# Performance work log

Measured on AMD Instinct MI355X. Metric: run time of the kernel, lower is better.

The kernel has to match this reference:

```python
import jax, jax.numpy as jnp
import numpy as np
from jax import lax

KERNEL = 2  # kernel_size, forced by the (s3-1, s4-1, s5-1) output reshape


def setup_inputs() -> dict:
    key = jax.random.key(0)
    kx, kw = jax.random.split(key)
    x = jax.random.normal(kx, (4, 16, 32, 32, 32), dtype=jnp.float32)
    w = jax.random.normal(kw, (512, 128), dtype=jnp.float32)  # (d1, d2=C*2^3)
    return {"x": x, "w": w}


def _gaussian_kernel(x, w):
    N, C, D, H, W = x.shape
    d1, d2 = w.shape
    # 3D unfold with kernel 2, stride 1, no padding -> (N, C*8, D-1, H-1, W-1)
    patches = lax.conv_general_dilated_patches(
        x,
        filter_shape=(KERNEL, KERNEL, KERNEL),
        window_strides=(1, 1, 1),
        padding='VALID',
    )
    P = (D - 1) * (H - 1) * (W - 1)
    y = patches.reshape(N, d2, P).transpose(0, 2, 1)  # (N, P, d2)
    # sum((y - w)^2) expanded as ||y||^2 - 2 y.w + ||w||^2 to avoid the
    # (N, P, d1, d2) broadcasted difference tensor.
    y_sq = jnp.sum(y * y, axis=-1, keepdims=True)           # (N, P, 1)
    w_sq = jnp.sum(w * w, axis=-1)                          # (d1,)
    cross = jnp.einsum('npd,kd->npk', y, w)                 # (N, P, d1)
    dist = y_sq - 2.0 * cross + w_sq                        # (N, P, d1)
    out = jnp.exp(-dist)
    return out.transpose(0, 2, 1).reshape(N, d1, D - 1, H - 1, W - 1)


def reference(x, w):
    return _gaussian_kernel(x, w)
```

## Files before the change

kernel.cpp:

```cpp
#include <hip/hip_runtime.h>

typedef unsigned short u16;
typedef unsigned char u8;
typedef float f32x4 __attribute__((ext_vector_type(4)));

#define P_OUT 29791
#define PPAD  29824
#define NBAT  4
#define NCH   512
#define KDIM  128

__device__ __forceinline__ unsigned pk4_fp8(float a, float b, float c, float d) {
  int v = __builtin_amdgcn_cvt_pk_fp8_f32(a, b, 0, false);
  v = __builtin_amdgcn_cvt_pk_fp8_f32(c, d, v, true);
  return (unsigned)v;
}

__global__ void prep_kernel(const float* __restrict__ x,
                            const float* __restrict__ w,
                            u8* __restrict__ yb, float* __restrict__ ysq,
                            u8* __restrict__ wb, float* __restrict__ wsq) {
  const int tid = threadIdx.x;
  const int b = blockIdx.x;
  if (b >= 3844) {
    const int g = (b - 3844) * 16 + (tid >> 4);
    const int c = tid & 15;
    const float4* wr = (const float4*)(w + g * 128 + c * 8);
    float4 f0 = wr[0], f1 = wr[1];
    float s = f0.x*f0.x + f0.y*f0.y + f0.z*f0.z + f0.w*f0.w
            + f1.x*f1.x + f1.y*f1.y + f1.z*f1.z + f1.w*f1.w;
#pragma unroll
    for (int m = 1; m < 16; m <<= 1) s += __shfl_xor(s, m, 64);
    uint2 pk;
    pk.x = pk4_fp8(f0.x, f0.y, f0.z, f0.w);
    pk.y = pk4_fp8(f1.x, f1.y, f1.z, f1.w);
    *(uint2*)(wb + g * 128 + c * 8) = pk;
    if (c == 0) wsq[g] = s;
    return;
  }
  __shared__ float xs[16][4][33];
  const int nb = b / 961;
  const int rem = b - nb * 961;
  const int d = rem / 31;
  const int h = rem - d * 31;
  const float* xb = x + ((size_t)nb << 19) + d * 1024 + h * 32;
#pragma unroll
  for (int t = 0; t < 8; ++t) {
    const int e = tid + 256 * t;
    const int c = e >> 7;
    const int r = (e >> 5) & 3;
    const int wv = e & 31;
    xs[c][r][wv] = xb[((size_t)c << 15) + (r >> 1) * 1024 + (r & 1) * 32 + wv];
  }
  __syncthreads();
  const int cs = tid & 15;
  const int wv0 = tid >> 4;
#pragma unroll
  for (int round = 0; round < 2; ++round) {
    const int wv = wv0 + 16 * round;
    if (wv <= 30) {
      const float v0 = xs[cs][0][wv], v1 = xs[cs][0][wv + 1];
      const float v2 = xs[cs][1][wv], v3 = xs[cs][1][wv + 1];
      const float v4 = xs[cs][2][wv], v5 = xs[cs][2][wv + 1];
      const float v6 = xs[cs][3][wv], v7 = xs[cs][3][wv + 1];
      float s = v0*v0 + v1*v1 + v2*v2 + v3*v3 + v4*v4 + v5*v5 + v6*v6 + v7*v7;
#pragma unroll
      for (int m = 1; m < 16; m <<= 1) s += __shfl_xor(s, m, 64);
      const int g = nb * PPAD + d * 961 + h * 31 + wv;
      uint2 pk;
      pk.x = pk4_fp8(v0, v1, v2, v3);
      pk.y = pk4_fp8(v4, v5, v6, v7);
      *(uint2*)(yb + (size_t)g * 128 + cs * 8) = pk;
      if (cs == 0) ysq[g] = s;
    }
  }
}

#define GLDS(g, l) __builtin_amdgcn_global_load_lds(                         \
    (const __attribute__((address_space(1))) unsigned int*)(g),              \
    (__attribute__((address_space(3))) unsigned int*)(l), 16, 0, 0)

__global__ void gauss_gemm_kernel(const u8* __restrict__ yb,
                                  const float* __restrict__ ysq,
                                  const u8* __restrict__ wb,
                                  const float* __restrict__ wsq,
                                  float* __restrict__ out) {
  __shared__ __align__(16) u8 Ws[128 * 128];
  __shared__ __align__(16) u8 Ys[128 * 128];

  const int bid = blockIdx.x;
  const int ct = bid & 3;
  const int pt = (bid >> 2) % 233;
  const int nb = bid / 932;
  const int p0 = pt * 128;
  const int c0 = ct * 128;

  const int tid = threadIdx.x;
  const int wid = tid >> 6;
  const int lane = tid & 63;
  const int quad = lane >> 4;
  const int col = lane & 15;
  const int wch = wid & 1;
  const int wp = wid >> 1;

  const size_t ybase = ((size_t)nb * PPAD + p0) * 128;

#pragma unroll
  for (int t = 0; t < 4; ++t) {
    const int Lb = (wid * 4 + t) * 64;
    const int L = Lb + lane;
    const int row = L >> 3;
    const int jc = (L & 7) ^ (row & 7);
    GLDS(wb + (size_t)(c0 + row) * 128 + jc * 16, &Ws[Lb * 16]);
    GLDS(yb + ybase + (size_t)row * 128 + jc * 16, &Ys[Lb * 16]);
  }

  f32x4 acc[4][4];
#pragma unroll
  for (int i = 0; i < 4; ++i)
#pragma unroll
    for (int j = 0; j < 4; ++j) acc[i][j] = (f32x4){0.f, 0.f, 0.f, 0.f};

  __syncthreads();

  const int c16b = quad >> 1;
  const int hoff = (quad & 1) * 8;
#pragma unroll
  for (int ks = 0; ks < 4; ++ks) {
    long long a[4], b[4];
#pragma unroll
    for (int i = 0; i < 4; ++i) {
      const int rowA = wch * 64 + i * 16 + col;
      const int pa = (ks * 2 + c16b) ^ (rowA & 7);
      a[i] = *(const long long*)&Ws[rowA * 128 + pa * 16 + hoff];
      const int rowB = wp * 64 + i * 16 + col;
      const int pb = (ks * 2 + c16b) ^ (rowB & 7);
      b[i] = *(const long long*)&Ys[rowB * 128 + pb * 16 + hoff];
    }
#pragma unroll
    for (int i = 0; i < 4; ++i)
#pragma unroll
      for (int j = 0; j < 4; ++j)
        acc[i][j] = __builtin_amdgcn_mfma_f32_16x16x32_fp8_fp8(a[i], b[j],
                                                               acc[i][j], 0, 0, 0);
  }

  float ysv[4];
  int pj[4];
#pragma unroll
  for (int j = 0; j < 4; ++j) {
    pj[j] = p0 + wp * 64 + j * 16 + col;
    ysv[j] = ysq[(size_t)nb * PPAD + pj[j]];
  }
#pragma unroll
  for (int i = 0; i < 4; ++i) {
#pragma unroll
    for (int r = 0; r < 4; ++r) {
      const int ch = c0 + wch * 64 + i * 16 + quad * 4 + r;
      const float wsv = wsq[ch];
      float* ob = out + ((size_t)(nb * NCH + ch)) * P_OUT;
#pragma unroll
      for (int j = 0; j < 4; ++j) {
        if (pj[j] < P_OUT) {
          const float dist = ysv[j] - 2.f * acc[i][j][r] + wsv;
          ob[pj[j]] = __expf(-dist);
        }
      }
    }
  }
}

extern "C" void kernel_launch(void* const* d_in, const int* in_sizes, int n_in,
                              void* d_out, int out_size, void* d_ws, size_t ws_size,
                              hipStream_t stream) {
  const float* x = (const float*)d_in[0];
  const float* w = (const float*)d_in[1];
  float* out = (float*)d_out;
  char* ws = (char*)d_ws;
  u8* yb     = (u8*)ws;
  float* ysq = (float*)(ws + 15269888);
  u8* wb     = (u8*)(ws + 15747072);
  float* wsq = (float*)(ws + 15812608);

  prep_kernel<<<3876, 256, 0, stream>>>(x, w, yb, ysq, wb, wsq);
  gauss_gemm_kernel<<<3728, 256, 0, stream>>>(yb, ysq, wb, wsq, out);
}
```

Before: 288.4 us.

## Make GEMM kernel persistent with resident W tile and prefetched Y tiles

Launches a fixed grid of 1024 blocks that loop over the 3728 output tiles. Each block keeps its W channel tile in LDS for all of its tiles, since the channel tile index is fixed per block. It issues the next Y tile's async global-to-LDS load before running the exp/store epilogue of the current tile. A separate unguarded store path handles full tiles. This aims to cut repeated W loads and block launch overhead and to hide Y load latency behind output stores, but it reduces the number of resident blocks available to keep the memory system busy.

```diff
diff --git a/kernel.cpp b/kernel.cpp
--- a/kernel.cpp
+++ b/kernel.cpp
@@ -9,6 +9,8 @@
 #define NBAT  4
 #define NCH   512
 #define KDIM  128
+#define NTILE 3728
+#define GRID  1024
 
 __device__ __forceinline__ unsigned pk4_fp8(float a, float b, float c, float d) {
   int v = __builtin_amdgcn_cvt_pk_fp8_f32(a, b, 0, false);
@@ -89,12 +91,6 @@
   __shared__ __align__(16) u8 Ys[128 * 128];
 
   const int bid = blockIdx.x;
-  const int ct = bid & 3;
-  const int pt = (bid >> 2) % 233;
-  const int nb = bid / 932;
-  const int p0 = pt * 128;
-  const int c0 = ct * 128;
-
   const int tid = threadIdx.x;
   const int wid = tid >> 6;
   const int lane = tid & 63;
@@ -103,7 +99,8 @@
   const int wch = wid & 1;
   const int wp = wid >> 1;
 
-  const size_t ybase = ((size_t)nb * PPAD + p0) * 128;
+  const int ct = bid & 3;
+  const int c0 = ct * 128;
 
 #pragma unroll
   for (int t = 0; t < 4; ++t) {
@@ -112,61 +109,118 @@
     const int row = L >> 3;
     const int jc = (L & 7) ^ (row & 7);
     GLDS(wb + (size_t)(c0 + row) * 128 + jc * 16, &Ws[Lb * 16]);
-    GLDS(yb + ybase + (size_t)row * 128 + jc * 16, &Ys[Lb * 16]);
-  }
-
-  f32x4 acc[4][4];
-#pragma unroll
-  for (int i = 0; i < 4; ++i)
-#pragma unroll
-    for (int j = 0; j < 4; ++j) acc[i][j] = (f32x4){0.f, 0.f, 0.f, 0.f};
+  }
+
+  int tile = bid;
+  int g0 = tile >> 2;
+  int nxt_nb = g0 / 233;
+  int nxt_pt = g0 - nxt_nb * 233;
+  {
+    const size_t yb2 = ((size_t)nxt_nb * PPAD + nxt_pt * 128) * 128;
+#pragma unroll
+    for (int t = 0; t < 4; ++t) {
+      const int Lb = (wid * 4 + t) * 64;
+      const int L = Lb + lane;
+      const int row = L >> 3;
+      const int jc = (L & 7) ^ (row & 7);
+      GLDS(yb + yb2 + (size_t)row * 128 + jc * 16, &Ys[Lb * 16]);
+    }
+  }
 
   __syncthreads();
 
   const int c16b = quad >> 1;
   const int hoff = (quad & 1) * 8;
-#pragma unroll
-  for (int ks = 0; ks < 4; ++ks) {
-    long long a[4], b[4];
-#pragma unroll
-    for (int i = 0; i < 4; ++i) {
-      const int rowA = wch * 64 + i * 16 + col;
-      const int pa = (ks * 2 + c16b) ^ (rowA & 7);
-      a[i] = *(const long long*)&Ws[rowA * 128 + pa * 16 + hoff];
-      const int rowB = wp * 64 + i * 16 + col;
-      const int pb = (ks * 2 + c16b) ^ (rowB & 7);
-      b[i] = *(const long long*)&Ys[rowB * 128 + pb * 16 + hoff];
-    }
+
+  for (;;) {
+    const int cur_nb = nxt_nb;
+    const int cur_p0 = nxt_pt * 128;
+
+    float ysv[4];
+    int pj[4];
+#pragma unroll
+    for (int j = 0; j < 4; ++j) {
+      pj[j] = cur_p0 + wp * 64 + j * 16 + col;
+      ysv[j] = ysq[(size_t)cur_nb * PPAD + pj[j]];
+    }
+
+    f32x4 acc[4][4];
 #pragma unroll
     for (int i = 0; i < 4; ++i)
 #pragma unroll
-      for (int j = 0; j < 4; ++j)
-        acc[i][j] = __builtin_amdgcn_mfma_f32_16x16x32_fp8_fp8(a[i], b[j],
-                                                               acc[i][j], 0, 0, 0);
-  }
-
-  float ysv[4];
-  int pj[4];
-#pragma unroll
-  for (int j = 0; j < 4; ++j) {
-    pj[j] = p0 + wp * 64 + j * 16 + col;
-    ysv[j] = ysq[(size_t)nb * PPAD + pj[j]];
-  }
-#pragma unroll
-  for (int i = 0; i < 4; ++i) {
-#pragma unroll
-    for (int r = 0; r < 4; ++r) {
-      const int ch = c0 + wch * 64 + i * 16 + quad * 4 + r;
-      const float wsv = wsq[ch];
-      float* ob = out + ((size_t)(nb * NCH + ch)) * P_OUT;
-#pragma unroll
-      for (int j = 0; j < 4; ++j) {
-        if (pj[j] < P_OUT) {
-          const float dist = ysv[j] - 2.f * acc[i][j][r] + wsv;
-          ob[pj[j]] = __expf(-dist);
+      for (int j = 0; j < 4; ++j) acc[i][j] = (f32x4){0.f, 0.f, 0.f, 0.f};
+
+#pragma unroll
+    for (int ks = 0; ks < 4; ++ks) {
+      long long a[4], b[4];
+#pragma unroll
+      for (int i = 0; i < 4; ++i) {
+        const int rowA = wch * 64 + i * 16 + col;
+        const int pa = (ks * 2 + c16b) ^ (rowA & 7);
+        a[i] = *(const long long*)&Ws[rowA * 128 + pa * 16 + hoff];
+        const int rowB = wp * 64 + i * 16 + col;
+        const int pb = (ks * 2 + c16b) ^ (rowB & 7);
+        b[i] = *(const long long*)&Ys[rowB * 128 + pb * 16 + hoff];
+      }
+#pragma unroll
+      for (int i = 0; i < 4; ++i)
+#pragma unroll
+        for (int j = 0; j < 4; ++j)
+          acc[i][j] = __builtin_amdgcn_mfma_f32_16x16x32_fp8_fp8(a[i], b[j],
+                                                                 acc[i][j], 0, 0, 0);
+    }
+
+    __syncthreads();
+
+    tile += GRID;
+    const bool has_next = (tile < NTILE);
+    if (has_next) {
+      const int gg = tile >> 2;
+      nxt_nb = gg / 233;
+      nxt_pt = gg - nxt_nb * 233;
+      const size_t yb2 = ((size_t)nxt_nb * PPAD + nxt_pt * 128) * 128;
+#pragma unroll
+      for (int t = 0; t < 4; ++t) {
+        const int Lb = (wid * 4 + t) * 64;
+        const int L = Lb + lane;
+        const int row = L >> 3;
+        const int jc = (L & 7) ^ (row & 7);
+        GLDS(yb + yb2 + (size_t)row * 128 + jc * 16, &Ys[Lb * 16]);
+      }
+    }
+
+    const bool full = (cur_p0 + 128 <= P_OUT);
+    if (full) {
+#pragma unroll
+      for (int i = 0; i < 4; ++i) {
+#pragma unroll
+        for (int r = 0; r < 4; ++r) {
+          const int ch = c0 + wch * 64 + i * 16 + quad * 4 + r;
+          const float wsv = wsq[ch];
+          float* ob = out + ((size_t)(cur_nb * NCH + ch)) * P_OUT;
+#pragma unroll
+          for (int j = 0; j < 4; ++j)
+            ob[pj[j]] = __expf(2.f * acc[i][j][r] - ysv[j] - wsv);
         }
       }
-    }
+    } else {
+#pragma unroll
+      for (int i = 0; i < 4; ++i) {
+#pragma unroll
+        for (int r = 0; r < 4; ++r) {
+          const int ch = c0 + wch * 64 + i * 16 + quad * 4 + r;
+          const float wsv = wsq[ch];
+          float* ob = out + ((size_t)(cur_nb * NCH + ch)) * P_OUT;
+#pragma unroll
+          for (int j = 0; j < 4; ++j)
+            if (pj[j] < P_OUT)
+              ob[pj[j]] = __expf(2.f * acc[i][j][r] - ysv[j] - wsv);
+        }
+      }
+    }
+
+    if (!has_next) break;
+    __syncthreads();
   }
 }
 
@@ -183,5 +237,5 @@
   float* wsq = (float*)(ws + 15812608);
 
   prep_kernel<<<3876, 256, 0, stream>>>(x, w, yb, ysq, wb, wsq);
-  gauss_gemm_kernel<<<3728, 256, 0, stream>>>(yb, ysq, wb, wsq, out);
-}
+  gauss_gemm_kernel<<<GRID, 256, 0, stream>>>(yb, ysq, wb, wsq, out);
+}
```

Measured after the change: 301.6 us. +4.6%, slower.

## Fuse 3D patch extraction and fp8 packing into the GEMM kernel

Applied to the files above, without the earlier changes.

Removes the separate prep pass that materialized fp8 patches and their squared norms in workspace. Each GEMM block now loads a raw x slab (16 channels x 2 depth planes x 5 h rows) into LDS and builds the fp8 B operands and row norms on the fly. Tiles are aligned to (d, 4 h-rows) groups with a swizzled block order, and launch bounds are added. This drops a full global write/read round trip and one launch, at the cost of extra per-block conversion ALU work and about 3% padding waste on partial h tiles.

```diff
diff --git a/kernel.cpp b/kernel.cpp
--- a/kernel.cpp
+++ b/kernel.cpp
@@ -1,14 +1,10 @@
 #include <hip/hip_runtime.h>
 
-typedef unsigned short u16;
 typedef unsigned char u8;
 typedef float f32x4 __attribute__((ext_vector_type(4)));
 
 #define P_OUT 29791
-#define PPAD  29824
-#define NBAT  4
 #define NCH   512
-#define KDIM  128
 
 __device__ __forceinline__ unsigned pk4_fp8(float a, float b, float c, float d) {
   int v = __builtin_amdgcn_cvt_pk_fp8_f32(a, b, 0, false);
@@ -16,84 +12,49 @@
   return (unsigned)v;
 }
 
-__global__ void prep_kernel(const float* __restrict__ x,
-                            const float* __restrict__ w,
-                            u8* __restrict__ yb, float* __restrict__ ysq,
-                            u8* __restrict__ wb, float* __restrict__ wsq) {
+__global__ void wprep_kernel(const float* __restrict__ w,
+                             u8* __restrict__ wb, float* __restrict__ wsq) {
   const int tid = threadIdx.x;
-  const int b = blockIdx.x;
-  if (b >= 3844) {
-    const int g = (b - 3844) * 16 + (tid >> 4);
-    const int c = tid & 15;
-    const float4* wr = (const float4*)(w + g * 128 + c * 8);
-    float4 f0 = wr[0], f1 = wr[1];
-    float s = f0.x*f0.x + f0.y*f0.y + f0.z*f0.z + f0.w*f0.w
-            + f1.x*f1.x + f1.y*f1.y + f1.z*f1.z + f1.w*f1.w;
+  const int g = blockIdx.x * 16 + (tid >> 4);
+  const int c = tid & 15;
+  const float4* wr = (const float4*)(w + g * 128 + c * 8);
+  float4 f0 = wr[0], f1 = wr[1];
+  float s = f0.x*f0.x + f0.y*f0.y + f0.z*f0.z + f0.w*f0.w
+          + f1.x*f1.x + f1.y*f1.y + f1.z*f1.z + f1.w*f1.w;
 #pragma unroll
-    for (int m = 1; m < 16; m <<= 1) s += __shfl_xor(s, m, 64);
-    uint2 pk;
-    pk.x = pk4_fp8(f0.x, f0.y, f0.z, f0.w);
-    pk.y = pk4_fp8(f1.x, f1.y, f1.z, f1.w);
-    *(uint2*)(wb + g * 128 + c * 8) = pk;
-    if (c == 0) wsq[g] = s;
-    return;
-  }
-  __shared__ float xs[16][4][33];
-  const int nb = b / 961;
-  const int rem = b - nb * 961;
-  const int d = rem / 31;
-  const int h = rem - d * 31;
-  const float* xb = x + ((size_t)nb << 19) + d * 1024 + h * 32;
-#pragma unroll
-  for (int t = 0; t < 8; ++t) {
-    const int e = tid + 256 * t;
-    const int c = e >> 7;
-    const int r = (e >> 5) & 3;
-    const int wv = e & 31;
-    xs[c][r][wv] = xb[((size_t)c << 15) + (r >> 1) * 1024 + (r & 1) * 32 + wv];
-  }
-  __syncthreads();
-  const int cs = tid & 15;
-  const int wv0 = tid >> 4;
-#pragma unroll
-  for (int round = 0; round < 2; ++round) {
-    const int wv = wv0 + 16 * round;
-    if (wv <= 30) {
-      const float v0 = xs[cs][0][wv], v1 = xs[cs][0][wv + 1];
-      const float v2 = xs[cs][1][wv], v3 = xs[cs][1][wv + 1];
-      const float v4 = xs[cs][2][wv], v5 = xs[cs][2][wv + 1];
-      const float v6 = xs[cs][3][wv], v7 = xs[cs][3][wv + 1];
-      float s = v0*v0 + v1*v1 + v2*v2 + v3*v3 + v4*v4 + v5*v5 + v6*v6 + v7*v7;
-#pragma unroll
-      for (int m = 1; m < 16; m <<= 1) s += __shfl_xor(s, m, 64);
-      const int g = nb * PPAD + d * 961 + h * 31 + wv;
-      uint2 pk;
-      pk.x = pk4_fp8(v0, v1, v2, v3);
-      pk.y = pk4_fp8(v4, v5, v6, v7);
-      *(uint2*)(yb + (size_t)g * 128 + cs * 8) = pk;
-      if (cs == 0) ysq[g] = s;
-    }
-  }
+  for (int m = 1; m < 16; m <<= 1) s += __shfl_xor(s, m, 64);
+  uint2 pk;
+  pk.x = pk4_fp8(f0.x, f0.y, f0.z, f0.w);
+  pk.y = pk4_fp8(f1.x, f1.y, f1.z, f1.w);
+  *(uint2*)(wb + g * 128 + c * 8) = pk;
+  if (c == 0) wsq[g] = s;
 }
 
 #define GLDS(g, l) __builtin_amdgcn_global_load_lds(                         \
     (const __attribute__((address_space(1))) unsigned int*)(g),              \
     (__attribute__((address_space(3))) unsigned int*)(l), 16, 0, 0)
 
-__global__ void gauss_gemm_kernel(const u8* __restrict__ yb,
-                                  const float* __restrict__ ysq,
-                                  const u8* __restrict__ wb,
-                                  const float* __restrict__ wsq,
-                                  float* __restrict__ out) {
+__global__ __launch_bounds__(256, 2)
+void gauss_fused_kernel(const float* __restrict__ x,
+                        const u8* __restrict__ wb,
+                        const float* __restrict__ wsq,
+                        float* __restrict__ out) {
   __shared__ __align__(16) u8 Ws[128 * 128];
-  __shared__ __align__(16) u8 Ys[128 * 128];
+  __shared__ __align__(16) float Xs[16 * 2 * 5 * 32];
 
   const int bid = blockIdx.x;
-  const int ct = bid & 3;
-  const int pt = (bid >> 2) % 233;
-  const int nb = bid / 932;
-  const int p0 = pt * 128;
+  const int tile = (bid & 7) * 496 + (bid >> 3);
+  const unsigned nb = (unsigned)tile / 992u;
+  const unsigned rem = (unsigned)tile - nb * 992u;
+  const unsigned ct = rem / 248u;
+  const unsigned r2 = rem - ct * 248u;
+  const unsigned d  = r2 >> 3;
+  const unsigned hb = r2 & 7;
+  const int h0 = hb * 4;
+  const int nh = (h0 + 4 <= 31) ? 4 : (31 - h0);
+  const int nrows = nh * 31;
   const int c0 = ct * 128;
+  const int tp0 = d * 961 + h0 * 31;
 
   const int tid = threadIdx.x;
   const int wid = tid >> 6;
@@ -103,8 +64,6 @@
   const int wch = wid & 1;
   const int wp = wid >> 1;
 
-  const size_t ybase = ((size_t)nb * PPAD + p0) * 128;
-
 #pragma unroll
   for (int t = 0; t < 4; ++t) {
     const int Lb = (wid * 4 + t) * 64;
@@ -112,7 +71,33 @@
     const int row = L >> 3;
     const int jc = (L & 7) ^ (row & 7);
     GLDS(wb + (size_t)(c0 + row) * 128 + jc * 16, &Ws[Lb * 16]);
-    GLDS(yb + ybase + (size_t)row * 128 + jc * 16, &Ys[Lb * 16]);
+  }
+
+#pragma unroll
+  for (int t = 0; t < 5; ++t) {
+    const int Lb = t * 256 + wid * 64;
+    const int L = Lb + lane;
+    const int row = L >> 3;
+    const int jc = L & 7;
+    const unsigned c = (unsigned)row / 10u;
+    const unsigned rr = (unsigned)row - c * 10u;
+    const unsigned kd = rr / 5u;
+    const unsigned hq = rr - kd * 5u;
+    const int hg = h0 + (int)hq;
+    const int hcl = (hg < 31) ? hg : 31;
+    GLDS(x + (((size_t)(nb * 16 + c)) << 15) + (d + kd) * 1024 + hcl * 32 + jc * 4,
+         &Xs[Lb * 4]);
+  }
+
+  int rb[4];
+  int xoff[4];
+#pragma unroll
+  for (int j = 0; j < 4; ++j) {
+    rb[j] = wp * 64 + j * 16 + col;
+    const unsigned rc = (unsigned)((rb[j] < nrows) ? rb[j] : (nrows - 1));
+    const unsigned hh = rc / 31u;
+    const unsigned wv = rc - hh * 31u;
+    xoff[j] = (int)(hh * 32 + wv);
   }
 
   f32x4 acc[4][4];
@@ -120,6 +105,8 @@
   for (int i = 0; i < 4; ++i)
 #pragma unroll
     for (int j = 0; j < 4; ++j) acc[i][j] = (f32x4){0.f, 0.f, 0.f, 0.f};
+
+  float sq[4] = {0.f, 0.f, 0.f, 0.f};
 
   __syncthreads();
 
@@ -133,9 +120,18 @@
       const int rowA = wch * 64 + i * 16 + col;
       const int pa = (ks * 2 + c16b) ^ (rowA & 7);
       a[i] = *(const long long*)&Ws[rowA * 128 + pa * 16 + hoff];
-      const int rowB = wp * 64 + i * 16 + col;
-      const int pb = (ks * 2 + c16b) ^ (rowB & 7);
-      b[i] = *(const long long*)&Ys[rowB * 128 + pb * 16 + hoff];
+    }
+    const int cc = ks * 4 + quad;
+    const float* xb = &Xs[cc * 320];
+#pragma unroll
+    for (int j = 0; j < 4; ++j) {
+      const float* pB = xb + xoff[j];
+      const float v0 = pB[0],   v1 = pB[1],   v2 = pB[32],  v3 = pB[33];
+      const float v4 = pB[160], v5 = pB[161], v6 = pB[192], v7 = pB[193];
+      sq[j] += v0*v0 + v1*v1 + v2*v2 + v3*v3 + v4*v4 + v5*v5 + v6*v6 + v7*v7;
+      const unsigned lo = pk4_fp8(v0, v1, v2, v3);
+      const unsigned hi = pk4_fp8(v4, v5, v6, v7);
+      b[j] = (long long)(((unsigned long long)hi << 32) | lo);
     }
 #pragma unroll
     for (int i = 0; i < 4; ++i)
@@ -145,13 +141,16 @@
                                                                acc[i][j], 0, 0, 0);
   }
 
-  float ysv[4];
+#pragma unroll
+  for (int j = 0; j < 4; ++j) {
+    sq[j] += __shfl_xor(sq[j], 16, 64);
+    sq[j] += __shfl_xor(sq[j], 32, 64);
+  }
+
   int pj[4];
 #pragma unroll
-  for (int j = 0; j < 4; ++j) {
-    pj[j] = p0 + wp * 64 + j * 16 + col;
-    ysv[j] = ysq[(size_t)nb * PPAD + pj[j]];
-  }
+  for (int j = 0; j < 4; ++j) pj[j] = tp0 + rb[j];
+
 #pragma unroll
   for (int i = 0; i < 4; ++i) {
 #pragma unroll
@@ -160,12 +159,9 @@
       const float wsv = wsq[ch];
       float* ob = out + ((size_t)(nb * NCH + ch)) * P_OUT;
 #pragma unroll
-      for (int j = 0; j < 4; ++j) {
-        if (pj[j] < P_OUT) {
-          const float dist = ysv[j] - 2.f * acc[i][j][r] + wsv;
-          ob[pj[j]] = __expf(-dist);
-        }
-      }
+      for (int j = 0; j < 4; ++j)
+        if (rb[j] < nrows)
+          ob[pj[j]] = __expf(2.f * acc[i][j][r] - sq[j] - wsv);
     }
   }
 }
@@ -177,11 +173,9 @@
   const float* w = (const float*)d_in[1];
   float* out = (float*)d_out;
   char* ws = (char*)d_ws;
-  u8* yb     = (u8*)ws;
-  float* ysq = (float*)(ws + 15269888);
-  u8* wb     = (u8*)(ws + 15747072);
-  float* wsq = (float*)(ws + 15812608);
+  u8* wb     = (u8*)ws;
+  float* wsq = (float*)(ws + 65536);
 
-  prep_kernel<<<3876, 256, 0, stream>>>(x, w, yb, ysq, wb, wsq);
-  gauss_gemm_kernel<<<3728, 256, 0, stream>>>(yb, ysq, wb, wsq, out);
+  wprep_kernel<<<32, 256, 0, stream>>>(w, wb, wsq);
+  gauss_fused_kernel<<<3968, 256, 0, stream>>>(x, wb, wsq, out);
 }
```

Result: faster. 268.7 us (-6.8%).
